# Optimization experiments

Measured on AMD Instinct MI355X. Metric: run time of the kernel, lower is better.

The kernel has to match this reference:

```python
import jax, jax.numpy as jnp
import numpy as np

N = 50000
D = 128
E = 600000


def setup_inputs() -> dict:
    key = jax.random.key(0)
    k1, k2, k3, k4, k5, k6 = jax.random.split(key, 6)
    x = jax.random.normal(k1, (N, D), dtype=jnp.float32)
    edge_index = jax.random.randint(k2, (2, E), 0, N, dtype=jnp.int32)
    s = 1.0 / np.sqrt(D)
    W1 = jax.random.uniform(k3, (D, D), dtype=jnp.float32, minval=-s, maxval=s)
    b1 = jax.random.uniform(k4, (D,), dtype=jnp.float32, minval=-s, maxval=s)
    W2 = jax.random.uniform(k5, (D, D), dtype=jnp.float32, minval=-s, maxval=s)
    b2 = jax.random.uniform(k6, (D,), dtype=jnp.float32, minval=-s, maxval=s)
    return {"x": x, "edge_index": edge_index, "W1": W1, "b1": b1, "W2": W2, "b2": b2}


def _gcn_conv(x, src, dst, W, b):
    # PyG GCNConv (default flow source->target): out[dst] += norm * (x @ W)[src] + b
    n = x.shape[0]
    deg = jax.ops.segment_sum(jnp.ones_like(dst, dtype=x.dtype), dst, num_segments=n)
    dinv = jnp.where(deg > 0, jax.lax.rsqrt(deg), 0.0)
    norm = dinv[src] * dinv[dst]          # [E+N]
    h = x @ W                             # [N, D]
    msg = h[src] * norm[:, None]          # [E+N, D] gather + scale
    out = jax.ops.segment_sum(msg, dst, num_segments=n)
    return out + b


def reference(x, edge_index, W1, b1, W2, b2):
    n = x.shape[0]
    loops = jnp.arange(n, dtype=edge_index.dtype)
    src = jnp.concatenate([edge_index[0], loops])  # add self-loops
    dst = jnp.concatenate([edge_index[1], loops])
    h = jax.nn.relu(_gcn_conv(x, src, dst, W1, b1))
    out = jax.nn.relu(_gcn_conv(h, src, dst, W2, b2))
    return out
```

## Files before the change

kernel.cpp:

```cpp
#include <hip/hip_runtime.h>
#include <stdint.h>

typedef __attribute__((ext_vector_type(8))) short bf16x8;
typedef __attribute__((ext_vector_type(4))) float f32x4;

#define CAP 64

__device__ __forceinline__ float bf2f(unsigned int u) {
    union { unsigned int i; float f; } v; v.i = u << 16; return v.f;
}
__device__ __forceinline__ unsigned int f2bf(float f) {
    union { float f; unsigned int i; } v; v.f = f;
    unsigned int b = v.i;
    b += 0x7FFFu + ((b >> 16) & 1u);
    return b >> 16;
}


__global__ void bucket_kernel(const int* __restrict__ src, const int* __restrict__ dst,
                              int* __restrict__ counts, unsigned short* __restrict__ bucket,
                              int E,
                              const float* __restrict__ W1, const float* __restrict__ W2,
                              unsigned short* __restrict__ Wt1, unsigned short* __restrict__ Wt2) {
    int t = blockIdx.x * 256 + threadIdx.x;
    if (t < 32768) {
        const float* W = (t < 16384) ? W1 : W2;
        unsigned short* O = (t < 16384) ? Wt1 : Wt2;
        int i = t & 16383;
        O[i] = (unsigned short)f2bf(W[(i & 127) * 128 + (i >> 7)]);
    }
    if (t < E) {
        int s = src[t], d = dst[t];
        int slot = atomicAdd(&counts[d], 1);
        if (slot < CAP) bucket[(size_t)d * CAP + slot] = (unsigned short)s;
    }
}


__global__ __launch_bounds__(256) void gemm128(const float* __restrict__ A,
                                               const unsigned short* __restrict__ Wt,
                                               const int* __restrict__ counts,
                                               unsigned short* __restrict__ bucket,
                                               unsigned short* __restrict__ G, int M) {
    int t = threadIdx.x;

    {
        int row = blockIdx.x * 64 + (t >> 2);
        if (row < M) {
            int deg = min(counts[row], CAP);
            int pe = (deg + 15) & ~15;
            if (pe < 16) pe = 16;
            for (int idx = deg + (t & 3); idx < pe; idx += 4)
                bucket[(size_t)row * CAP + idx] = (unsigned short)M;
        }
    }
    if (blockIdx.x == 0 && t < 64)
        ((unsigned int*)G)[(size_t)M * 64 + t] = 0u;

    int wave = t >> 6, lane = t & 63;
    int m0 = (blockIdx.x * 4 + wave) * 16;
    int mrow = lane & 15, quad = lane >> 4;

    int arow = m0 + mrow;
    int srow = arow < M ? arow : M - 1;
    const float* Arow = A + (size_t)srow * 128;

    f32x4 acc[8];
#pragma unroll
    for (int nt = 0; nt < 8; ++nt) acc[nt] = (f32x4){0.f, 0.f, 0.f, 0.f};

#pragma unroll
    for (int kb = 0; kb < 4; ++kb) {
        f32x4 lo = *(const f32x4*)(Arow + kb * 32 + quad * 8);
        f32x4 hi = *(const f32x4*)(Arow + kb * 32 + quad * 8 + 4);
        bf16x8 a;
#pragma unroll
        for (int i = 0; i < 4; ++i) { a[i] = (short)f2bf(lo[i]); a[i + 4] = (short)f2bf(hi[i]); }
#pragma unroll
        for (int nt = 0; nt < 8; ++nt) {
            bf16x8 b = *(const bf16x8*)(Wt + (size_t)(nt * 16 + mrow) * 128 + kb * 32 + quad * 8);
            acc[nt] = __builtin_amdgcn_mfma_f32_16x16x32_bf16(a, b, acc[nt], 0, 0, 0);
        }
    }

#pragma unroll
    for (int r = 0; r < 4; ++r) {
        int row = m0 + quad * 4 + r;
        if (row < M) {
            float dr = rsqrtf((float)counts[row] + 1.0f);
#pragma unroll
            for (int nt = 0; nt < 8; ++nt)
                G[(size_t)row * 128 + nt * 16 + mrow] = (unsigned short)f2bf(acc[nt][r] * dr);
        }
    }
}


template <bool FINAL>
__global__ __launch_bounds__(256) void agg_kernel(const unsigned short* __restrict__ g,
                                                  const int* __restrict__ counts,
                                                  const unsigned short* __restrict__ bucket,
                                                  const float* __restrict__ bias,
                                                  const unsigned short* __restrict__ Wt,
                                                  unsigned short* __restrict__ G2,
                                                  float* __restrict__ outf,
                                                  int N) {
    __shared__ __align__(16) unsigned short As[FINAL ? 1 : 16][136];
    int wave = threadIdx.x >> 6, lane = threadIdx.x & 63;
    const unsigned int* g32 = (const unsigned int*)g;
    int nb0 = blockIdx.x * 16 + wave * 4;

    if (!FINAL && blockIdx.x == 0 && threadIdx.x < 64)
        ((unsigned int*)G2)[(size_t)N * 64 + threadIdx.x] = 0u;

    int degs[4]; unsigned int svs[4]; unsigned int hvs[4];
#pragma unroll
    for (int i = 0; i < 4; ++i) {
        int n = min(nb0 + i, N - 1);
        degs[i] = counts[n];
        svs[i]  = bucket[(size_t)n * CAP + lane];
        hvs[i]  = g32[(size_t)n * 64 + lane];
    }
    float2 bv = ((const float2*)bias)[lane];

    unsigned int vv[4][16];
#pragma unroll
    for (int i = 0; i < 4; ++i) {
#pragma unroll
        for (int u = 0; u < 16; ++u) {
            int s = __builtin_amdgcn_readlane(svs[i], u);
            vv[i][u] = *(g32 + (size_t)s * 64 + lane);
        }
    }

#pragma unroll
    for (int i = 0; i < 4; ++i) {
        int deg = degs[i];
        int m = min(deg, CAP);
        int mr = (m + 15) & ~15;
        if (mr < 16) mr = 16;
        float di = rsqrtf((float)deg + 1.0f);
        float a0 = bf2f(hvs[i] & 0xFFFFu);
        float a1 = bf2f(hvs[i] >> 16);
        float c0 = 0.f, c1 = 0.f;
#pragma unroll
        for (int u = 0; u < 16; ++u) {
            unsigned int v = vv[i][u];
            if (u & 1) { c0 += bf2f(v & 0xFFFFu); c1 += bf2f(v >> 16); }
            else       { a0 += bf2f(v & 0xFFFFu); a1 += bf2f(v >> 16); }
        }
#pragma unroll 1
        for (int j0 = 16; j0 < mr; j0 += 16) {
            unsigned int v2[16];
#pragma unroll
            for (int u = 0; u < 16; ++u) {
                int s = __builtin_amdgcn_readlane(svs[i], j0 + u);
                v2[u] = *(g32 + (size_t)s * 64 + lane);
            }
#pragma unroll
            for (int u = 0; u < 16; ++u) {
                unsigned int v = v2[u];
                if (u & 1) { c0 += bf2f(v & 0xFFFFu); c1 += bf2f(v >> 16); }
                else       { a0 += bf2f(v & 0xFFFFu); a1 += bf2f(v >> 16); }
            }
        }
        float o0 = fmaxf((a0 + c0) * di + bv.x, 0.f);
        float o1 = fmaxf((a1 + c1) * di + bv.y, 0.f);
        if (FINAL) {
            int n = nb0 + i;
            if (n < N) ((float2*)outf)[(size_t)n * 64 + lane] = make_float2(o0, o1);
        } else {
            *(unsigned int*)&As[wave * 4 + i][lane * 2] = f2bf(o0) | (f2bf(o1) << 16);
        }
    }

    if (FINAL) return;

    __syncthreads();

    int mrow = lane & 15, quad = lane >> 4;
    f32x4 acc[2];
    acc[0] = (f32x4){0.f, 0.f, 0.f, 0.f};
    acc[1] = (f32x4){0.f, 0.f, 0.f, 0.f};
#pragma unroll
    for (int kb = 0; kb < 4; ++kb) {
        bf16x8 a = *(const bf16x8*)(&As[mrow][kb * 32 + quad * 8]);
#pragma unroll
        for (int q = 0; q < 2; ++q) {
            int nt = wave * 2 + q;
            bf16x8 b = *(const bf16x8*)(Wt + (size_t)(nt * 16 + mrow) * 128 + kb * 32 + quad * 8);
            acc[q] = __builtin_amdgcn_mfma_f32_16x16x32_bf16(a, b, acc[q], 0, 0, 0);
        }
    }
#pragma unroll
    for (int r = 0; r < 4; ++r) {
        int row = blockIdx.x * 16 + quad * 4 + r;
        if (row < N) {
            float dr = rsqrtf((float)counts[row] + 1.0f);
#pragma unroll
            for (int q = 0; q < 2; ++q) {
                int nt = wave * 2 + q;
                G2[(size_t)row * 128 + nt * 16 + mrow] = (unsigned short)f2bf(acc[q][r] * dr);
            }
        }
    }
}


extern "C" void kernel_launch(void* const* d_in, const int* in_sizes, int n_in,
                              void* d_out, int out_size, void* d_ws, size_t ws_size,
                              hipStream_t stream) {
    const float* x  = (const float*)d_in[0];
    const int*   ei = (const int*)d_in[1];
    const float* W1 = (const float*)d_in[2];
    const float* b1 = (const float*)d_in[3];
    const float* W2 = (const float*)d_in[4];
    const float* b2 = (const float*)d_in[5];
    float* out = (float*)d_out;

    int N = in_sizes[0] / 128;
    int E = in_sizes[1] / 2;
    const int* src = ei;
    const int* dst = ei + E;

    char* p = (char*)d_ws;
    auto alloc = [&](size_t bytes) {
        char* r = p; p += (bytes + 255) & ~(size_t)255; return r;
    };
    int*            counts = (int*)           alloc((size_t)N * 4);
    unsigned short* bucket = (unsigned short*)alloc((size_t)N * CAP * 2);
    unsigned short* g1     = (unsigned short*)alloc((size_t)(N + 1) * 128 * 2);
    unsigned short* g2     = (unsigned short*)alloc((size_t)(N + 1) * 128 * 2);
    unsigned short* Wt1    = (unsigned short*)alloc(16384 * 2);
    unsigned short* Wt2    = (unsigned short*)alloc(16384 * 2);

    hipMemsetAsync(counts, 0, (size_t)N * 4, stream);
    bucket_kernel<<<(E + 255) / 256, 256, 0, stream>>>(src, dst, counts, bucket, E,
                                                       W1, W2, Wt1, Wt2);

    gemm128<<<(N + 63) / 64, 256, 0, stream>>>(x, Wt1, counts, bucket, g1, N);
    agg_kernel<false><<<(N + 15) / 16, 256, 0, stream>>>(g1, counts, bucket, b1, Wt2, g2, nullptr, N);
    agg_kernel<true ><<<(N + 15) / 16, 256, 0, stream>>>(g2, counts, bucket, b2, nullptr, nullptr, out, N);
}
```

Before: 192.8 us.

## Fuse all GCN stages into one persistent cooperative kernel with grid syncs

Replaces the four separate launches (bucketing, first GEMM, fused aggregate+GEMM, final aggregate) with one cooperative persistent kernel. Grid-stride loops cover each stage and grid.sync() separates them. The aim is to remove per-launch overhead and inter-kernel gaps. In exchange, occupancy is capped by cooperative residency, grid-wide barriers add cost, and the heavy register use in the aggregation loops may limit blocks per CU.

```diff
diff --git a/kernel.cpp b/kernel.cpp
--- a/kernel.cpp
+++ b/kernel.cpp
@@ -1,5 +1,8 @@
 #include <hip/hip_runtime.h>
+#include <hip/hip_cooperative_groups.h>
 #include <stdint.h>
+
+namespace cg = cooperative_groups;
 
 typedef __attribute__((ext_vector_type(8))) short bf16x8;
 typedef __attribute__((ext_vector_type(4))) float f32x4;
@@ -17,191 +20,241 @@
 }
 
 
-__global__ void bucket_kernel(const int* __restrict__ src, const int* __restrict__ dst,
-                              int* __restrict__ counts, unsigned short* __restrict__ bucket,
-                              int E,
-                              const float* __restrict__ W1, const float* __restrict__ W2,
-                              unsigned short* __restrict__ Wt1, unsigned short* __restrict__ Wt2) {
-    int t = blockIdx.x * 256 + threadIdx.x;
-    if (t < 32768) {
-        const float* W = (t < 16384) ? W1 : W2;
-        unsigned short* O = (t < 16384) ? Wt1 : Wt2;
-        int i = t & 16383;
-        O[i] = (unsigned short)f2bf(W[(i & 127) * 128 + (i >> 7)]);
-    }
-    if (t < E) {
-        int s = src[t], d = dst[t];
+__global__ __launch_bounds__(256) void mega(
+    const int* __restrict__ src, const int* __restrict__ dst, int E,
+    const float* __restrict__ x,
+    const float* __restrict__ W1, const float* __restrict__ b1,
+    const float* __restrict__ W2, const float* __restrict__ b2,
+    int* __restrict__ counts, unsigned short* __restrict__ bucket,
+    unsigned short* __restrict__ g1, unsigned short* __restrict__ g2,
+    unsigned short* __restrict__ Wt1, unsigned short* __restrict__ Wt2,
+    float* __restrict__ out, int N)
+{
+    __shared__ __align__(16) unsigned short As[16][136];
+    cg::grid_group grid = cg::this_grid();
+
+    const int t    = threadIdx.x;
+    const int gid  = blockIdx.x * 256 + t;
+    const int gsz  = gridDim.x * 256;
+    const int wave = t >> 6, lane = t & 63;
+
+    for (int i = gid; i < 32768; i += gsz) {
+        const float* W = (i < 16384) ? W1 : W2;
+        unsigned short* O = (i < 16384) ? Wt1 : Wt2;
+        int j = i & 16383;
+        O[j] = (unsigned short)f2bf(W[(j & 127) * 128 + (j >> 7)]);
+    }
+    for (int e = gid; e < E; e += gsz) {
+        int s = src[e], d = dst[e];
         int slot = atomicAdd(&counts[d], 1);
         if (slot < CAP) bucket[(size_t)d * CAP + slot] = (unsigned short)s;
     }
-}
-
-
-__global__ __launch_bounds__(256) void gemm128(const float* __restrict__ A,
-                                               const unsigned short* __restrict__ Wt,
-                                               const int* __restrict__ counts,
-                                               unsigned short* __restrict__ bucket,
-                                               unsigned short* __restrict__ G, int M) {
-    int t = threadIdx.x;
-
-    {
-        int row = blockIdx.x * 64 + (t >> 2);
-        if (row < M) {
-            int deg = min(counts[row], CAP);
-            int pe = (deg + 15) & ~15;
-            if (pe < 16) pe = 16;
-            for (int idx = deg + (t & 3); idx < pe; idx += 4)
-                bucket[(size_t)row * CAP + idx] = (unsigned short)M;
-        }
-    }
-    if (blockIdx.x == 0 && t < 64)
-        ((unsigned int*)G)[(size_t)M * 64 + t] = 0u;
-
-    int wave = t >> 6, lane = t & 63;
-    int m0 = (blockIdx.x * 4 + wave) * 16;
-    int mrow = lane & 15, quad = lane >> 4;
-
-    int arow = m0 + mrow;
-    int srow = arow < M ? arow : M - 1;
-    const float* Arow = A + (size_t)srow * 128;
-
-    f32x4 acc[8];
-#pragma unroll
-    for (int nt = 0; nt < 8; ++nt) acc[nt] = (f32x4){0.f, 0.f, 0.f, 0.f};
-
-#pragma unroll
-    for (int kb = 0; kb < 4; ++kb) {
-        f32x4 lo = *(const f32x4*)(Arow + kb * 32 + quad * 8);
-        f32x4 hi = *(const f32x4*)(Arow + kb * 32 + quad * 8 + 4);
-        bf16x8 a;
-#pragma unroll
-        for (int i = 0; i < 4; ++i) { a[i] = (short)f2bf(lo[i]); a[i + 4] = (short)f2bf(hi[i]); }
-#pragma unroll
-        for (int nt = 0; nt < 8; ++nt) {
-            bf16x8 b = *(const bf16x8*)(Wt + (size_t)(nt * 16 + mrow) * 128 + kb * 32 + quad * 8);
-            acc[nt] = __builtin_amdgcn_mfma_f32_16x16x32_bf16(a, b, acc[nt], 0, 0, 0);
-        }
-    }
-
-#pragma unroll
-    for (int r = 0; r < 4; ++r) {
-        int row = m0 + quad * 4 + r;
-        if (row < M) {
-            float dr = rsqrtf((float)counts[row] + 1.0f);
-#pragma unroll
-            for (int nt = 0; nt < 8; ++nt)
-                G[(size_t)row * 128 + nt * 16 + mrow] = (unsigned short)f2bf(acc[nt][r] * dr);
-        }
-    }
-}
-
-
-template <bool FINAL>
-__global__ __launch_bounds__(256) void agg_kernel(const unsigned short* __restrict__ g,
-                                                  const int* __restrict__ counts,
-                                                  const unsigned short* __restrict__ bucket,
-                                                  const float* __restrict__ bias,
-                                                  const unsigned short* __restrict__ Wt,
-                                                  unsigned short* __restrict__ G2,
-                                                  float* __restrict__ outf,
-                                                  int N) {
-    __shared__ __align__(16) unsigned short As[FINAL ? 1 : 16][136];
-    int wave = threadIdx.x >> 6, lane = threadIdx.x & 63;
-    const unsigned int* g32 = (const unsigned int*)g;
-    int nb0 = blockIdx.x * 16 + wave * 4;
-
-    if (!FINAL && blockIdx.x == 0 && threadIdx.x < 64)
-        ((unsigned int*)G2)[(size_t)N * 64 + threadIdx.x] = 0u;
-
-    int degs[4]; unsigned int svs[4]; unsigned int hvs[4];
-#pragma unroll
-    for (int i = 0; i < 4; ++i) {
-        int n = min(nb0 + i, N - 1);
-        degs[i] = counts[n];
-        svs[i]  = bucket[(size_t)n * CAP + lane];
-        hvs[i]  = g32[(size_t)n * 64 + lane];
-    }
-    float2 bv = ((const float2*)bias)[lane];
-
-    unsigned int vv[4][16];
-#pragma unroll
-    for (int i = 0; i < 4; ++i) {
-#pragma unroll
-        for (int u = 0; u < 16; ++u) {
-            int s = __builtin_amdgcn_readlane(svs[i], u);
-            vv[i][u] = *(g32 + (size_t)s * 64 + lane);
-        }
-    }
-
-#pragma unroll
-    for (int i = 0; i < 4; ++i) {
-        int deg = degs[i];
-        int m = min(deg, CAP);
-        int mr = (m + 15) & ~15;
-        if (mr < 16) mr = 16;
-        float di = rsqrtf((float)deg + 1.0f);
-        float a0 = bf2f(hvs[i] & 0xFFFFu);
-        float a1 = bf2f(hvs[i] >> 16);
-        float c0 = 0.f, c1 = 0.f;
-#pragma unroll
-        for (int u = 0; u < 16; ++u) {
-            unsigned int v = vv[i][u];
-            if (u & 1) { c0 += bf2f(v & 0xFFFFu); c1 += bf2f(v >> 16); }
-            else       { a0 += bf2f(v & 0xFFFFu); a1 += bf2f(v >> 16); }
-        }
-#pragma unroll 1
-        for (int j0 = 16; j0 < mr; j0 += 16) {
-            unsigned int v2[16];
+
+    grid.sync();
+
+    if (blockIdx.x == 0) {
+        if (t < 64)       ((unsigned int*)g1)[(size_t)N * 64 + t]        = 0u;
+        else if (t < 128) ((unsigned int*)g2)[(size_t)N * 64 + (t - 64)] = 0u;
+    }
+    const int mrow = lane & 15, quad = lane >> 4;
+    int ntile = (N + 63) >> 6;
+    for (int tile = blockIdx.x; tile < ntile; tile += gridDim.x) {
+        {
+            int row = tile * 64 + (t >> 2);
+            if (row < N) {
+                int deg = min(counts[row], CAP);
+                int pe = (deg + 15) & ~15;
+                if (pe < 16) pe = 16;
+                for (int idx = deg + (t & 3); idx < pe; idx += 4)
+                    bucket[(size_t)row * CAP + idx] = (unsigned short)N;
+            }
+        }
+        int m0 = (tile * 4 + wave) * 16;
+        int arow = m0 + mrow;
+        int srow = arow < N ? arow : N - 1;
+        const float* Arow = x + (size_t)srow * 128;
+
+        f32x4 acc[8];
+#pragma unroll
+        for (int nt = 0; nt < 8; ++nt) acc[nt] = (f32x4){0.f, 0.f, 0.f, 0.f};
+#pragma unroll
+        for (int kb = 0; kb < 4; ++kb) {
+            f32x4 lo = *(const f32x4*)(Arow + kb * 32 + quad * 8);
+            f32x4 hi = *(const f32x4*)(Arow + kb * 32 + quad * 8 + 4);
+            bf16x8 a;
+#pragma unroll
+            for (int i = 0; i < 4; ++i) { a[i] = (short)f2bf(lo[i]); a[i + 4] = (short)f2bf(hi[i]); }
+#pragma unroll
+            for (int nt = 0; nt < 8; ++nt) {
+                bf16x8 b = *(const bf16x8*)(Wt1 + (size_t)(nt * 16 + mrow) * 128 + kb * 32 + quad * 8);
+                acc[nt] = __builtin_amdgcn_mfma_f32_16x16x32_bf16(a, b, acc[nt], 0, 0, 0);
+            }
+        }
+#pragma unroll
+        for (int r = 0; r < 4; ++r) {
+            int row = m0 + quad * 4 + r;
+            if (row < N) {
+                float dr = rsqrtf((float)counts[row] + 1.0f);
+#pragma unroll
+                for (int nt = 0; nt < 8; ++nt)
+                    g1[(size_t)row * 128 + nt * 16 + mrow] = (unsigned short)f2bf(acc[nt][r] * dr);
+            }
+        }
+    }
+
+    grid.sync();
+
+    int ngrp = (N + 15) >> 4;
+    for (int grp = blockIdx.x; grp < ngrp; grp += gridDim.x) {
+        const unsigned int* g32 = (const unsigned int*)g1;
+        int nb0 = grp * 16 + wave * 4;
+
+        int degs[4]; unsigned int svs[4]; unsigned int hvs[4];
+#pragma unroll
+        for (int i = 0; i < 4; ++i) {
+            int n = min(nb0 + i, N - 1);
+            degs[i] = counts[n];
+            svs[i]  = bucket[(size_t)n * CAP + lane];
+            hvs[i]  = g32[(size_t)n * 64 + lane];
+        }
+        float2 bv = ((const float2*)b1)[lane];
+
+        unsigned int vv[4][16];
+#pragma unroll
+        for (int i = 0; i < 4; ++i) {
 #pragma unroll
             for (int u = 0; u < 16; ++u) {
-                int s = __builtin_amdgcn_readlane(svs[i], j0 + u);
-                v2[u] = *(g32 + (size_t)s * 64 + lane);
-            }
+                int s = __builtin_amdgcn_readlane(svs[i], u);
+                vv[i][u] = *(g32 + (size_t)s * 64 + lane);
+            }
+        }
+
+#pragma unroll
+        for (int i = 0; i < 4; ++i) {
+            int deg = degs[i];
+            int m = min(deg, CAP);
+            int mr = (m + 15) & ~15;
+            if (mr < 16) mr = 16;
+            float di = rsqrtf((float)deg + 1.0f);
+            float a0 = bf2f(hvs[i] & 0xFFFFu);
+            float a1 = bf2f(hvs[i] >> 16);
+            float c0 = 0.f, c1 = 0.f;
 #pragma unroll
             for (int u = 0; u < 16; ++u) {
-                unsigned int v = v2[u];
+                unsigned int v = vv[i][u];
                 if (u & 1) { c0 += bf2f(v & 0xFFFFu); c1 += bf2f(v >> 16); }
                 else       { a0 += bf2f(v & 0xFFFFu); a1 += bf2f(v >> 16); }
             }
-        }
-        float o0 = fmaxf((a0 + c0) * di + bv.x, 0.f);
-        float o1 = fmaxf((a1 + c1) * di + bv.y, 0.f);
-        if (FINAL) {
-            int n = nb0 + i;
-            if (n < N) ((float2*)outf)[(size_t)n * 64 + lane] = make_float2(o0, o1);
-        } else {
+#pragma unroll 1
+            for (int j0 = 16; j0 < mr; j0 += 16) {
+                unsigned int v2[16];
+#pragma unroll
+                for (int u = 0; u < 16; ++u) {
+                    int s = __builtin_amdgcn_readlane(svs[i], j0 + u);
+                    v2[u] = *(g32 + (size_t)s * 64 + lane);
+                }
+#pragma unroll
+                for (int u = 0; u < 16; ++u) {
+                    unsigned int v = v2[u];
+                    if (u & 1) { c0 += bf2f(v & 0xFFFFu); c1 += bf2f(v >> 16); }
+                    else       { a0 += bf2f(v & 0xFFFFu); a1 += bf2f(v >> 16); }
+                }
+            }
+            float o0 = fmaxf((a0 + c0) * di + bv.x, 0.f);
+            float o1 = fmaxf((a1 + c1) * di + bv.y, 0.f);
             *(unsigned int*)&As[wave * 4 + i][lane * 2] = f2bf(o0) | (f2bf(o1) << 16);
         }
-    }
-
-    if (FINAL) return;
-
-    __syncthreads();
-
-    int mrow = lane & 15, quad = lane >> 4;
-    f32x4 acc[2];
-    acc[0] = (f32x4){0.f, 0.f, 0.f, 0.f};
-    acc[1] = (f32x4){0.f, 0.f, 0.f, 0.f};
-#pragma unroll
-    for (int kb = 0; kb < 4; ++kb) {
-        bf16x8 a = *(const bf16x8*)(&As[mrow][kb * 32 + quad * 8]);
-#pragma unroll
-        for (int q = 0; q < 2; ++q) {
-            int nt = wave * 2 + q;
-            bf16x8 b = *(const bf16x8*)(Wt + (size_t)(nt * 16 + mrow) * 128 + kb * 32 + quad * 8);
-            acc[q] = __builtin_amdgcn_mfma_f32_16x16x32_bf16(a, b, acc[q], 0, 0, 0);
-        }
-    }
-#pragma unroll
-    for (int r = 0; r < 4; ++r) {
-        int row = blockIdx.x * 16 + quad * 4 + r;
-        if (row < N) {
-            float dr = rsqrtf((float)counts[row] + 1.0f);
+        __syncthreads();
+
+        f32x4 acc[2];
+        acc[0] = (f32x4){0.f, 0.f, 0.f, 0.f};
+        acc[1] = (f32x4){0.f, 0.f, 0.f, 0.f};
+#pragma unroll
+        for (int kb = 0; kb < 4; ++kb) {
+            bf16x8 a = *(const bf16x8*)(&As[mrow][kb * 32 + quad * 8]);
 #pragma unroll
             for (int q = 0; q < 2; ++q) {
                 int nt = wave * 2 + q;
-                G2[(size_t)row * 128 + nt * 16 + mrow] = (unsigned short)f2bf(acc[q][r] * dr);
-            }
+                bf16x8 b = *(const bf16x8*)(Wt2 + (size_t)(nt * 16 + mrow) * 128 + kb * 32 + quad * 8);
+                acc[q] = __builtin_amdgcn_mfma_f32_16x16x32_bf16(a, b, acc[q], 0, 0, 0);
+            }
+        }
+#pragma unroll
+        for (int r = 0; r < 4; ++r) {
+            int row = grp * 16 + quad * 4 + r;
+            if (row < N) {
+                float dr = rsqrtf((float)counts[row] + 1.0f);
+#pragma unroll
+                for (int q = 0; q < 2; ++q) {
+                    int nt = wave * 2 + q;
+                    g2[(size_t)row * 128 + nt * 16 + mrow] = (unsigned short)f2bf(acc[q][r] * dr);
+                }
+            }
+        }
+        __syncthreads();
+    }
+
+    grid.sync();
+
+    for (int grp = blockIdx.x; grp < ngrp; grp += gridDim.x) {
+        const unsigned int* g32 = (const unsigned int*)g2;
+        int nb0 = grp * 16 + wave * 4;
+
+        int degs[4]; unsigned int svs[4]; unsigned int hvs[4];
+#pragma unroll
+        for (int i = 0; i < 4; ++i) {
+            int n = min(nb0 + i, N - 1);
+            degs[i] = counts[n];
+            svs[i]  = bucket[(size_t)n * CAP + lane];
+            hvs[i]  = g32[(size_t)n * 64 + lane];
+        }
+        float2 bv = ((const float2*)b2)[lane];
+
+        unsigned int vv[4][16];
+#pragma unroll
+        for (int i = 0; i < 4; ++i) {
+#pragma unroll
+            for (int u = 0; u < 16; ++u) {
+                int s = __builtin_amdgcn_readlane(svs[i], u);
+                vv[i][u] = *(g32 + (size_t)s * 64 + lane);
+            }
+        }
+
+#pragma unroll
+        for (int i = 0; i < 4; ++i) {
+            int deg = degs[i];
+            int m = min(deg, CAP);
+            int mr = (m + 15) & ~15;
+            if (mr < 16) mr = 16;
+            float di = rsqrtf((float)deg + 1.0f);
+            float a0 = bf2f(hvs[i] & 0xFFFFu);
+            float a1 = bf2f(hvs[i] >> 16);
+            float c0 = 0.f, c1 = 0.f;
+#pragma unroll
+            for (int u = 0; u < 16; ++u) {
+                unsigned int v = vv[i][u];
+                if (u & 1) { c0 += bf2f(v & 0xFFFFu); c1 += bf2f(v >> 16); }
+                else       { a0 += bf2f(v & 0xFFFFu); a1 += bf2f(v >> 16); }
+            }
+#pragma unroll 1
+            for (int j0 = 16; j0 < mr; j0 += 16) {
+                unsigned int v2[16];
+#pragma unroll
+                for (int u = 0; u < 16; ++u) {
+                    int s = __builtin_amdgcn_readlane(svs[i], j0 + u);
+                    v2[u] = *(g32 + (size_t)s * 64 + lane);
+                }
+#pragma unroll
+                for (int u = 0; u < 16; ++u) {
+                    unsigned int v = v2[u];
+                    if (u & 1) { c0 += bf2f(v & 0xFFFFu); c1 += bf2f(v >> 16); }
+                    else       { a0 += bf2f(v & 0xFFFFu); a1 += bf2f(v >> 16); }
+                }
+            }
+            float o0 = fmaxf((a0 + c0) * di + bv.x, 0.f);
+            float o1 = fmaxf((a1 + c1) * di + bv.y, 0.f);
+            int n = nb0 + i;
+            if (n < N) ((float2*)out)[(size_t)n * 64 + lane] = make_float2(o0, o1);
         }
     }
 }
@@ -234,11 +287,28 @@
     unsigned short* Wt1    = (unsigned short*)alloc(16384 * 2);
     unsigned short* Wt2    = (unsigned short*)alloc(16384 * 2);
 
+    static int gridBlocks = 0;
+    if (gridBlocks == 0) {
+        int dev = 0;
+        hipGetDevice(&dev);
+        hipDeviceProp_t prop;
+        hipGetDeviceProperties(&prop, dev);
+        int maxB = 0;
+        hipError_t err = hipOccupancyMaxActiveBlocksPerMultiprocessor(&maxB, (const void*)mega, 256, 0);
+        if (err != hipSuccess || maxB < 1) maxB = 2;
+        gridBlocks = prop.multiProcessorCount * maxB;
+        if (gridBlocks > 3136) gridBlocks = 3136;
+        if (gridBlocks < 1) gridBlocks = 256;
+    }
+
     hipMemsetAsync(counts, 0, (size_t)N * 4, stream);
-    bucket_kernel<<<(E + 255) / 256, 256, 0, stream>>>(src, dst, counts, bucket, E,
-                                                       W1, W2, Wt1, Wt2);
-
-    gemm128<<<(N + 63) / 64, 256, 0, stream>>>(x, Wt1, counts, bucket, g1, N);
-    agg_kernel<false><<<(N + 15) / 16, 256, 0, stream>>>(g1, counts, bucket, b1, Wt2, g2, nullptr, N);
-    agg_kernel<true ><<<(N + 15) / 16, 256, 0, stream>>>(g2, counts, bucket, b2, nullptr, nullptr, out, N);
+
+    void* args[] = {
+        (void*)&src, (void*)&dst, (void*)&E,
+        (void*)&x, (void*)&W1, (void*)&b1, (void*)&W2, (void*)&b2,
+        (void*)&counts, (void*)&bucket, (void*)&g1, (void*)&g2,
+        (void*)&Wt1, (void*)&Wt2, (void*)&out, (void*)&N
+    };
+    hipLaunchCooperativeKernel((const void*)mega, dim3(gridBlocks), dim3(256),
+                               args, 0, stream);
 }
```

Result: slower. 340.5 us (+76.6%).

## Make aggregation kernel persistent over node groups with software-pipelined gathers

Applied to the files above, without the earlier changes.

Each aggregation block now handles GPB groups of 16 nodes instead of one. It prefetches the next group's counts, bucket entries and neighbour rows while it finishes the current group's reduction and the fused MFMA transform. The W2 fragments are loaded into registers once per block, and the per-row dinv values are kept in shared memory rather than recomputed from counts. This trades fewer blocks, and so less latency hiding from occupancy, and higher register pressure for overlap of the gather latency with compute.

```diff
diff --git a/kernel.cpp b/kernel.cpp
--- a/kernel.cpp
+++ b/kernel.cpp
@@ -5,6 +5,7 @@
 typedef __attribute__((ext_vector_type(4))) float f32x4;
 
 #define CAP 64
+#define GPB 4
 
 __device__ __forceinline__ float bf2f(unsigned int u) {
     union { unsigned int i; float f; } v; v.i = u << 16; return v.f;
@@ -43,6 +44,8 @@
                                                unsigned short* __restrict__ bucket,
                                                unsigned short* __restrict__ G, int M) {
     int t = threadIdx.x;
+    int wave = t >> 6, lane = t & 63;
+    int mrow = lane & 15, quad = lane >> 4;
 
     {
         int row = blockIdx.x * 64 + (t >> 2);
@@ -57,10 +60,7 @@
     if (blockIdx.x == 0 && t < 64)
         ((unsigned int*)G)[(size_t)M * 64 + t] = 0u;
 
-    int wave = t >> 6, lane = t & 63;
     int m0 = (blockIdx.x * 4 + wave) * 16;
-    int mrow = lane & 15, quad = lane >> 4;
-
     int arow = m0 + mrow;
     int srow = arow < M ? arow : M - 1;
     const float* Arow = A + (size_t)srow * 128;
@@ -106,102 +106,154 @@
                                                   float* __restrict__ outf,
                                                   int N) {
     __shared__ __align__(16) unsigned short As[FINAL ? 1 : 16][136];
+    __shared__ float dinv_s[FINAL ? 1 : 16];
     int wave = threadIdx.x >> 6, lane = threadIdx.x & 63;
     const unsigned int* g32 = (const unsigned int*)g;
-    int nb0 = blockIdx.x * 16 + wave * 4;
+    int mrow = lane & 15, quad = lane >> 4;
+    int ngrp = (N + 15) >> 4;
+    int grp0 = blockIdx.x * GPB;
+    if (grp0 >= ngrp) return;
 
     if (!FINAL && blockIdx.x == 0 && threadIdx.x < 64)
         ((unsigned int*)G2)[(size_t)N * 64 + threadIdx.x] = 0u;
 
-    int degs[4]; unsigned int svs[4]; unsigned int hvs[4];
-#pragma unroll
-    for (int i = 0; i < 4; ++i) {
-        int n = min(nb0 + i, N - 1);
-        degs[i] = counts[n];
-        svs[i]  = bucket[(size_t)n * CAP + lane];
-        hvs[i]  = g32[(size_t)n * 64 + lane];
-    }
     float2 bv = ((const float2*)bias)[lane];
 
+    bf16x8 bfr[8];
+    if (!FINAL) {
+#pragma unroll
+        for (int kb = 0; kb < 4; ++kb)
+#pragma unroll
+            for (int q = 0; q < 2; ++q) {
+                int nt = wave * 2 + q;
+                bfr[kb * 2 + q] = *(const bf16x8*)(Wt + (size_t)(nt * 16 + mrow) * 128 + kb * 32 + quad * 8);
+            }
+    }
+
+    int degs[4]; unsigned int svs[4], hvs[4];
     unsigned int vv[4][16];
-#pragma unroll
-    for (int i = 0; i < 4; ++i) {
-#pragma unroll
-        for (int u = 0; u < 16; ++u) {
-            int s = __builtin_amdgcn_readlane(svs[i], u);
-            vv[i][u] = *(g32 + (size_t)s * 64 + lane);
-        }
-    }
-
-#pragma unroll
-    for (int i = 0; i < 4; ++i) {
-        int deg = degs[i];
-        int m = min(deg, CAP);
-        int mr = (m + 15) & ~15;
-        if (mr < 16) mr = 16;
-        float di = rsqrtf((float)deg + 1.0f);
-        float a0 = bf2f(hvs[i] & 0xFFFFu);
-        float a1 = bf2f(hvs[i] >> 16);
-        float c0 = 0.f, c1 = 0.f;
-#pragma unroll
-        for (int u = 0; u < 16; ++u) {
-            unsigned int v = vv[i][u];
-            if (u & 1) { c0 += bf2f(v & 0xFFFFu); c1 += bf2f(v >> 16); }
-            else       { a0 += bf2f(v & 0xFFFFu); a1 += bf2f(v >> 16); }
-        }
+
+    {
+        int nb0 = grp0 * 16 + wave * 4;
+#pragma unroll
+        for (int i = 0; i < 4; ++i) {
+            int n = min(nb0 + i, N - 1);
+            degs[i] = counts[n];
+            svs[i]  = bucket[(size_t)n * CAP + lane];
+            hvs[i]  = g32[(size_t)n * 64 + lane];
+        }
+#pragma unroll
+        for (int i = 0; i < 4; ++i)
+#pragma unroll
+            for (int u = 0; u < 16; ++u) {
+                int s = __builtin_amdgcn_readlane(svs[i], u);
+                vv[i][u] = g32[(size_t)s * 64 + lane];
+            }
+    }
+
 #pragma unroll 1
-        for (int j0 = 16; j0 < mr; j0 += 16) {
-            unsigned int v2[16];
+    for (int it = 0; it < GPB; ++it) {
+        int grp = grp0 + it;
+        if (grp >= ngrp) break;
+        bool hasnxt = (it + 1 < GPB) && (grp + 1 < ngrp);
+
+        int degs2[4]; unsigned int svs2[4], hvs2[4];
+
+#pragma unroll
+        for (int i = 0; i < 4; ++i) {
+            int deg = degs[i];
+            int m = min(deg, CAP);
+            int mr = (m + 15) & ~15;
+            if (mr < 16) mr = 16;
+            float di = rsqrtf((float)deg + 1.0f);
+            float a0 = bf2f(hvs[i] & 0xFFFFu);
+            float a1 = bf2f(hvs[i] >> 16);
+            float c0 = 0.f, c1 = 0.f;
 #pragma unroll
             for (int u = 0; u < 16; ++u) {
-                int s = __builtin_amdgcn_readlane(svs[i], j0 + u);
-                v2[u] = *(g32 + (size_t)s * 64 + lane);
-            }
-#pragma unroll
-            for (int u = 0; u < 16; ++u) {
-                unsigned int v = v2[u];
+                unsigned int v = vv[i][u];
                 if (u & 1) { c0 += bf2f(v & 0xFFFFu); c1 += bf2f(v >> 16); }
                 else       { a0 += bf2f(v & 0xFFFFu); a1 += bf2f(v >> 16); }
             }
-        }
-        float o0 = fmaxf((a0 + c0) * di + bv.x, 0.f);
-        float o1 = fmaxf((a1 + c1) * di + bv.y, 0.f);
-        if (FINAL) {
-            int n = nb0 + i;
-            if (n < N) ((float2*)outf)[(size_t)n * 64 + lane] = make_float2(o0, o1);
-        } else {
-            *(unsigned int*)&As[wave * 4 + i][lane * 2] = f2bf(o0) | (f2bf(o1) << 16);
-        }
-    }
-
-    if (FINAL) return;
-
-    __syncthreads();
-
-    int mrow = lane & 15, quad = lane >> 4;
-    f32x4 acc[2];
-    acc[0] = (f32x4){0.f, 0.f, 0.f, 0.f};
-    acc[1] = (f32x4){0.f, 0.f, 0.f, 0.f};
-#pragma unroll
-    for (int kb = 0; kb < 4; ++kb) {
-        bf16x8 a = *(const bf16x8*)(&As[mrow][kb * 32 + quad * 8]);
-#pragma unroll
-        for (int q = 0; q < 2; ++q) {
-            int nt = wave * 2 + q;
-            bf16x8 b = *(const bf16x8*)(Wt + (size_t)(nt * 16 + mrow) * 128 + kb * 32 + quad * 8);
-            acc[q] = __builtin_amdgcn_mfma_f32_16x16x32_bf16(a, b, acc[q], 0, 0, 0);
-        }
-    }
-#pragma unroll
-    for (int r = 0; r < 4; ++r) {
-        int row = blockIdx.x * 16 + quad * 4 + r;
-        if (row < N) {
-            float dr = rsqrtf((float)counts[row] + 1.0f);
-#pragma unroll
-            for (int q = 0; q < 2; ++q) {
-                int nt = wave * 2 + q;
-                G2[(size_t)row * 128 + nt * 16 + mrow] = (unsigned short)f2bf(acc[q][r] * dr);
-            }
+#pragma unroll 1
+            for (int j0 = 16; j0 < mr; j0 += 16) {
+                unsigned int v2[16];
+#pragma unroll
+                for (int u = 0; u < 16; ++u) {
+                    int s = __builtin_amdgcn_readlane(svs[i], j0 + u);
+                    v2[u] = g32[(size_t)s * 64 + lane];
+                }
+#pragma unroll
+                for (int u = 0; u < 16; ++u) {
+                    unsigned int v = v2[u];
+                    if (u & 1) { c0 += bf2f(v & 0xFFFFu); c1 += bf2f(v >> 16); }
+                    else       { a0 += bf2f(v & 0xFFFFu); a1 += bf2f(v >> 16); }
+                }
+            }
+            float o0 = fmaxf((a0 + c0) * di + bv.x, 0.f);
+            float o1 = fmaxf((a1 + c1) * di + bv.y, 0.f);
+            if (FINAL) {
+                int n = grp * 16 + wave * 4 + i;
+                if (n < N) ((float2*)outf)[(size_t)n * 64 + lane] = make_float2(o0, o1);
+            } else {
+                *(unsigned int*)&As[wave * 4 + i][lane * 2] = f2bf(o0) | (f2bf(o1) << 16);
+                if (lane == 0) dinv_s[wave * 4 + i] = di;
+            }
+
+            if (i == 0 && hasnxt) {
+                __builtin_amdgcn_sched_barrier(0);
+                int nb1 = (grp + 1) * 16 + wave * 4;
+#pragma unroll
+                for (int k = 0; k < 4; ++k) {
+                    int n = min(nb1 + k, N - 1);
+                    degs2[k] = counts[n];
+                    svs2[k]  = bucket[(size_t)n * CAP + lane];
+                    hvs2[k]  = g32[(size_t)n * 64 + lane];
+                }
+                __builtin_amdgcn_sched_barrier(0);
+            }
+        }
+
+        if (hasnxt) {
+#pragma unroll
+            for (int i = 0; i < 4; ++i)
+#pragma unroll
+                for (int u = 0; u < 16; ++u) {
+                    int s = __builtin_amdgcn_readlane(svs2[i], u);
+                    vv[i][u] = g32[(size_t)s * 64 + lane];
+                }
+        }
+
+        if (!FINAL) {
+            asm volatile("s_waitcnt lgkmcnt(0)\n\ts_barrier" ::: "memory");
+
+            f32x4 acc[2];
+            acc[0] = (f32x4){0.f, 0.f, 0.f, 0.f};
+            acc[1] = (f32x4){0.f, 0.f, 0.f, 0.f};
+#pragma unroll
+            for (int kb = 0; kb < 4; ++kb) {
+                bf16x8 a = *(const bf16x8*)(&As[mrow][kb * 32 + quad * 8]);
+                acc[0] = __builtin_amdgcn_mfma_f32_16x16x32_bf16(a, bfr[kb * 2 + 0], acc[0], 0, 0, 0);
+                acc[1] = __builtin_amdgcn_mfma_f32_16x16x32_bf16(a, bfr[kb * 2 + 1], acc[1], 0, 0, 0);
+            }
+#pragma unroll
+            for (int r = 0; r < 4; ++r) {
+                int row = grp * 16 + quad * 4 + r;
+                if (row < N) {
+                    float dr = dinv_s[quad * 4 + r];
+#pragma unroll
+                    for (int q = 0; q < 2; ++q) {
+                        int nt = wave * 2 + q;
+                        G2[(size_t)row * 128 + nt * 16 + mrow] = (unsigned short)f2bf(acc[q][r] * dr);
+                    }
+                }
+            }
+            asm volatile("s_waitcnt lgkmcnt(0)\n\ts_barrier" ::: "memory");
+        }
+
+        if (hasnxt) {
+#pragma unroll
+            for (int i = 0; i < 4; ++i) { degs[i] = degs2[i]; svs[i] = svs2[i]; hvs[i] = hvs2[i]; }
         }
     }
 }
@@ -238,7 +290,9 @@
     bucket_kernel<<<(E + 255) / 256, 256, 0, stream>>>(src, dst, counts, bucket, E,
                                                        W1, W2, Wt1, Wt2);
 
+    int ngrp = (N + 15) / 16;
+    int ablk = (ngrp + GPB - 1) / GPB;
     gemm128<<<(N + 63) / 64, 256, 0, stream>>>(x, Wt1, counts, bucket, g1, N);
-    agg_kernel<false><<<(N + 15) / 16, 256, 0, stream>>>(g1, counts, bucket, b1, Wt2, g2, nullptr, N);
-    agg_kernel<true ><<<(N + 15) / 16, 256, 0, stream>>>(g2, counts, bucket, b2, nullptr, nullptr, out, N);
-}
+    agg_kernel<false><<<ablk, 256, 0, stream>>>(g1, counts, bucket, b1, Wt2, g2, nullptr, N);
+    agg_kernel<true ><<<ablk, 256, 0, stream>>>(g2, counts, bucket, b2, nullptr, nullptr, out, N);
+}
```

Result: slower. 204.8 us (+6.2%).

## Gather neighbor rows with 16-byte loads across lane groups, fold self-loop into bucket

Applied to the files above, without the earlier changes.

The aggregation kernel now loads each neighbor row as 16-byte chunks, so each 64-lane wave gathers 4 neighbors per load instruction instead of one 4-byte word per lane per neighbor. It then reduces the partial sums across the lane groups with xor shuffles. The self-loop is stored as slot 0 of each node's bucket instead of being loaded separately. This cuts the number of gather instructions and raises bytes per request, at the cost of cross-lane shuffle reductions and one fewer usable bucket slot for real edges.

```diff
diff --git a/kernel.cpp b/kernel.cpp
--- a/kernel.cpp
+++ b/kernel.cpp
@@ -32,7 +32,7 @@
     if (t < E) {
         int s = src[t], d = dst[t];
         int slot = atomicAdd(&counts[d], 1);
-        if (slot < CAP) bucket[(size_t)d * CAP + slot] = (unsigned short)s;
+        if (slot < CAP - 1) bucket[(size_t)d * CAP + slot + 1] = (unsigned short)s;
     }
 }
 
@@ -43,24 +43,23 @@
                                                unsigned short* __restrict__ bucket,
                                                unsigned short* __restrict__ G, int M) {
     int t = threadIdx.x;
+    int wave = t >> 6, lane = t & 63;
+    int mrow = lane & 15, quad = lane >> 4;
 
     {
         int row = blockIdx.x * 64 + (t >> 2);
         if (row < M) {
-            int deg = min(counts[row], CAP);
-            int pe = (deg + 15) & ~15;
-            if (pe < 16) pe = 16;
-            for (int idx = deg + (t & 3); idx < pe; idx += 4)
+            int rows = 1 + min(counts[row], CAP - 1);
+            int pe = (rows + 15) & ~15;
+            if ((t & 3) == 0) bucket[(size_t)row * CAP] = (unsigned short)row;
+            for (int idx = rows + (t & 3); idx < pe; idx += 4)
                 bucket[(size_t)row * CAP + idx] = (unsigned short)M;
         }
     }
     if (blockIdx.x == 0 && t < 64)
         ((unsigned int*)G)[(size_t)M * 64 + t] = 0u;
 
-    int wave = t >> 6, lane = t & 63;
     int m0 = (blockIdx.x * 4 + wave) * 16;
-    int mrow = lane & 15, quad = lane >> 4;
-
     int arow = m0 + mrow;
     int srow = arow < M ? arow : M - 1;
     const float* Arow = A + (size_t)srow * 128;
@@ -107,70 +106,100 @@
                                                   int N) {
     __shared__ __align__(16) unsigned short As[FINAL ? 1 : 16][136];
     int wave = threadIdx.x >> 6, lane = threadIdx.x & 63;
-    const unsigned int* g32 = (const unsigned int*)g;
+    int p = lane & 15, grp = lane >> 4;
+    const char* gb = (const char*)g;
     int nb0 = blockIdx.x * 16 + wave * 4;
 
     if (!FINAL && blockIdx.x == 0 && threadIdx.x < 64)
         ((unsigned int*)G2)[(size_t)N * 64 + threadIdx.x] = 0u;
 
-    int degs[4]; unsigned int svs[4]; unsigned int hvs[4];
+    float4 bva = ((const float4*)bias)[p * 2];
+    float4 bvb = ((const float4*)bias)[p * 2 + 1];
+
+    int degs[4]; unsigned int svs[4];
 #pragma unroll
     for (int i = 0; i < 4; ++i) {
         int n = min(nb0 + i, N - 1);
         degs[i] = counts[n];
         svs[i]  = bucket[(size_t)n * CAP + lane];
-        hvs[i]  = g32[(size_t)n * 64 + lane];
-    }
-    float2 bv = ((const float2*)bias)[lane];
-
-    unsigned int vv[4][16];
-#pragma unroll
-    for (int i = 0; i < 4; ++i) {
-#pragma unroll
-        for (int u = 0; u < 16; ++u) {
-            int s = __builtin_amdgcn_readlane(svs[i], u);
-            vv[i][u] = *(g32 + (size_t)s * 64 + lane);
-        }
-    }
+    }
+
+    uint4 vq[4][4];
+#pragma unroll
+    for (int i = 0; i < 4; ++i)
+#pragma unroll
+        for (int q = 0; q < 4; ++q) {
+            int s = __shfl((int)svs[i], 4 * q + grp);
+            vq[i][q] = *(const uint4*)(gb + (size_t)s * 256 + p * 16);
+        }
 
 #pragma unroll
     for (int i = 0; i < 4; ++i) {
         int deg = degs[i];
-        int m = min(deg, CAP);
-        int mr = (m + 15) & ~15;
-        if (mr < 16) mr = 16;
+        int rows = 1 + min(deg, CAP - 1);
+        int mr = (rows + 15) & ~15;
         float di = rsqrtf((float)deg + 1.0f);
-        float a0 = bf2f(hvs[i] & 0xFFFFu);
-        float a1 = bf2f(hvs[i] >> 16);
-        float c0 = 0.f, c1 = 0.f;
-#pragma unroll
-        for (int u = 0; u < 16; ++u) {
-            unsigned int v = vv[i][u];
-            if (u & 1) { c0 += bf2f(v & 0xFFFFu); c1 += bf2f(v >> 16); }
-            else       { a0 += bf2f(v & 0xFFFFu); a1 += bf2f(v >> 16); }
-        }
+        float acc[8];
+#pragma unroll
+        for (int k = 0; k < 8; ++k) acc[k] = 0.f;
+#pragma unroll
+        for (int q = 0; q < 4; ++q)
+#pragma unroll
+            for (int d = 0; d < 4; ++d) {
+                unsigned int v = (&vq[i][q].x)[d];
+                acc[d * 2]     += bf2f(v & 0xFFFFu);
+                acc[d * 2 + 1] += bf2f(v >> 16);
+            }
 #pragma unroll 1
         for (int j0 = 16; j0 < mr; j0 += 16) {
-            unsigned int v2[16];
-#pragma unroll
-            for (int u = 0; u < 16; ++u) {
-                int s = __builtin_amdgcn_readlane(svs[i], j0 + u);
-                v2[u] = *(g32 + (size_t)s * 64 + lane);
-            }
-#pragma unroll
-            for (int u = 0; u < 16; ++u) {
-                unsigned int v = v2[u];
-                if (u & 1) { c0 += bf2f(v & 0xFFFFu); c1 += bf2f(v >> 16); }
-                else       { a0 += bf2f(v & 0xFFFFu); a1 += bf2f(v >> 16); }
-            }
-        }
-        float o0 = fmaxf((a0 + c0) * di + bv.x, 0.f);
-        float o1 = fmaxf((a1 + c1) * di + bv.y, 0.f);
+            uint4 tq[4];
+#pragma unroll
+            for (int q = 0; q < 4; ++q) {
+                int s = __shfl((int)svs[i], j0 + 4 * q + grp);
+                tq[q] = *(const uint4*)(gb + (size_t)s * 256 + p * 16);
+            }
+#pragma unroll
+            for (int q = 0; q < 4; ++q)
+#pragma unroll
+                for (int d = 0; d < 4; ++d) {
+                    unsigned int v = (&tq[q].x)[d];
+                    acc[d * 2]     += bf2f(v & 0xFFFFu);
+                    acc[d * 2 + 1] += bf2f(v >> 16);
+                }
+        }
+#pragma unroll
+        for (int k = 0; k < 8; ++k) {
+            acc[k] += __shfl_xor(acc[k], 16);
+            acc[k] += __shfl_xor(acc[k], 32);
+        }
+        float o[8];
+        o[0] = fmaxf(acc[0] * di + bva.x, 0.f);
+        o[1] = fmaxf(acc[1] * di + bva.y, 0.f);
+        o[2] = fmaxf(acc[2] * di + bva.z, 0.f);
+        o[3] = fmaxf(acc[3] * di + bva.w, 0.f);
+        o[4] = fmaxf(acc[4] * di + bvb.x, 0.f);
+        o[5] = fmaxf(acc[5] * di + bvb.y, 0.f);
+        o[6] = fmaxf(acc[6] * di + bvb.z, 0.f);
+        o[7] = fmaxf(acc[7] * di + bvb.w, 0.f);
+
         if (FINAL) {
-            int n = nb0 + i;
-            if (n < N) ((float2*)outf)[(size_t)n * 64 + lane] = make_float2(o0, o1);
+            if (grp == i) {
+                int n = nb0 + i;
+                if (n < N) {
+                    float4* op = (float4*)(outf + (size_t)n * 128 + p * 8);
+                    op[0] = make_float4(o[0], o[1], o[2], o[3]);
+                    op[1] = make_float4(o[4], o[5], o[6], o[7]);
+                }
+            }
         } else {
-            *(unsigned int*)&As[wave * 4 + i][lane * 2] = f2bf(o0) | (f2bf(o1) << 16);
+            if (grp == i) {
+                uint4 w;
+                w.x = f2bf(o[0]) | (f2bf(o[1]) << 16);
+                w.y = f2bf(o[2]) | (f2bf(o[3]) << 16);
+                w.z = f2bf(o[4]) | (f2bf(o[5]) << 16);
+                w.w = f2bf(o[6]) | (f2bf(o[7]) << 16);
+                *(uint4*)&As[wave * 4 + i][p * 8] = w;
+            }
         }
     }
 
@@ -179,9 +208,9 @@
     __syncthreads();
 
     int mrow = lane & 15, quad = lane >> 4;
-    f32x4 acc[2];
-    acc[0] = (f32x4){0.f, 0.f, 0.f, 0.f};
-    acc[1] = (f32x4){0.f, 0.f, 0.f, 0.f};
+    f32x4 acc2[2];
+    acc2[0] = (f32x4){0.f, 0.f, 0.f, 0.f};
+    acc2[1] = (f32x4){0.f, 0.f, 0.f, 0.f};
 #pragma unroll
     for (int kb = 0; kb < 4; ++kb) {
         bf16x8 a = *(const bf16x8*)(&As[mrow][kb * 32 + quad * 8]);
@@ -189,7 +218,7 @@
         for (int q = 0; q < 2; ++q) {
             int nt = wave * 2 + q;
             bf16x8 b = *(const bf16x8*)(Wt + (size_t)(nt * 16 + mrow) * 128 + kb * 32 + quad * 8);
-            acc[q] = __builtin_amdgcn_mfma_f32_16x16x32_bf16(a, b, acc[q], 0, 0, 0);
+            acc2[q] = __builtin_amdgcn_mfma_f32_16x16x32_bf16(a, b, acc2[q], 0, 0, 0);
         }
     }
 #pragma unroll
@@ -200,7 +229,7 @@
 #pragma unroll
             for (int q = 0; q < 2; ++q) {
                 int nt = wave * 2 + q;
-                G2[(size_t)row * 128 + nt * 16 + mrow] = (unsigned short)f2bf(acc[q][r] * dr);
+                G2[(size_t)row * 128 + nt * 16 + mrow] = (unsigned short)f2bf(acc2[q][r] * dr);
             }
         }
     }
```

Measured after the change: 194.5 us. Within noise of the previous version (+0.9%).
